# Kernel tuning notes

Hardware: AMD Instinct MI355X
Metric: run time of the kernel (lower is better)

## Reference

```python
import jax, jax.numpy as jnp
import numpy as np

NUM_CLS = 80
SR = 0.2
STRIDES = (8, 16, 32, 64, 128)
IMG = 1280
FMAPS = [(IMG // s, IMG // s) for s in STRIDES]
MAX_BOXES = 128
BIG_AREA = 1e7  # padding value for box-area argmin (matches tf.pad constant)


def _shrink_boxes(boxes, fw, fh, stride, sr):
    # shrink gt boxes by `sr` around their center and snap to feature-grid ints
    b = boxes / stride
    cx = (b[:, 0] + b[:, 2]) * 0.5
    cy = (b[:, 1] + b[:, 3]) * 0.5
    hw = (b[:, 2] - b[:, 0]) * sr * 0.5
    hh = (b[:, 3] - b[:, 1]) * sr * 0.5
    px1 = jnp.clip(jnp.floor(cx - hw), 0, fw - 1).astype(jnp.int32)
    py1 = jnp.clip(jnp.floor(cy - hh), 0, fh - 1).astype(jnp.int32)
    px2 = jnp.clip(jnp.ceil(cx + hw).astype(jnp.int32), px1 + 1, fw)
    py2 = jnp.clip(jnp.ceil(cy + hh).astype(jnp.int32), py1 + 1, fh)
    return px1, py1, px2, py2


def _level_targets(boxes, labels, valid, sel_w, fh, fw, stride):
    # Vectorized replacement of the per-box tf.map_fn + tf.pad + argmin + gather_nd.
    # The original builds a padded dense map per box; padding values are:
    #   cls one-hot -> 0, soft weight -> 1, regr mask -> 0, regr target -> 0, area -> 1e7.
    # We instead compute dense [K,fh,fw] maps and mask, which is the same math.
    px1, py1, px2, py2 = _shrink_boxes(boxes, fw, fh, stride, SR)  # [K]
    sx = (jnp.arange(fw, dtype=jnp.float32) + 0.5) * stride  # pixel-center x
    sy = (jnp.arange(fh, dtype=jnp.float32) + 0.5) * stride  # pixel-center y
    dl = jnp.maximum(sx[None, None, :] - boxes[:, 0, None, None], 0.0)  # [K,fh,fw]
    dt = jnp.maximum(sy[None, :, None] - boxes[:, 1, None, None], 0.0)
    dr = jnp.maximum(boxes[:, 2, None, None] - sx[None, None, :], 0.0)
    db = jnp.maximum(boxes[:, 3, None, None] - sy[None, :, None], 0.0)
    gx = jnp.arange(fw)[None, None, :]
    gy = jnp.arange(fh)[None, :, None]
    in_box = ((gx >= px1[:, None, None]) & (gx < px2[:, None, None])
              & (gy >= py1[:, None, None]) & (gy < py2[:, None, None])
              & valid[:, None, None])  # [K,fh,fw] positive region per box
    area = jnp.where(in_box, (dl + dr) * (dt + db), BIG_AREA)
    win = jnp.argmin(area, axis=0)  # [fh,fw] smallest-area box per pixel

    take = lambda a: jnp.take_along_axis(a, win[None], axis=0)[0]
    is_pos = take(in_box).astype(jnp.float32)
    dl_w, dt_w, dr_w, db_w = take(dl), take(dt), take(dr), take(db)

    # anchor-point weight min/max ratio (guard 0/0 which is only hit off-target)
    num = jnp.minimum(dl_w, dr_w) * jnp.minimum(dt_w, db_w)
    den = jnp.maximum(dl_w, dr_w) * jnp.maximum(dt_w, db_w)
    ap = jnp.where(den > 0, num / jnp.maximum(den, 1e-12), 0.0)
    soft = jnp.where(is_pos > 0, ap * sel_w[win], 1.0)

    onehot = jax.nn.one_hot(labels[win], NUM_CLS, dtype=jnp.float32) * is_pos[..., None]
    regr = (jnp.stack([dl_w, dt_w, dr_w, db_w], axis=-1) / (4.0 * stride)) * is_pos[..., None]
    extra = jnp.stack([soft, is_pos], axis=-1)  # [fh,fw,2] soft weight + pos mask
    cls_t = jnp.concatenate([onehot, extra], axis=-1).reshape(fh * fw, NUM_CLS + 2)
    regr_t = jnp.concatenate([regr, extra], axis=-1).reshape(fh * fw, 4 + 2)
    return cls_t, regr_t


def reference(gt_boxes, feature_select_weight, feature_maps_shape):
    # feature_maps_shape is accepted for signature fidelity; shapes must be
    # static under jit so we use the FMAPS constant (same values).
    labels = gt_boxes[:, 4].astype(jnp.int32)
    boxes = gt_boxes[:, :4]
    valid = jnp.any(jnp.abs(boxes) > 0, axis=1)  # trim_zero_padding_boxes as mask
    cls_list, regr_list = [], []
    for lvl, stride in enumerate(STRIDES):
        fh, fw = FMAPS[lvl]
        c, r = _level_targets(boxes, labels, valid,
                              feature_select_weight[:, lvl], fh, fw, stride)
        cls_list.append(c)
        regr_list.append(r)
    return jnp.concatenate(cls_list, axis=0), jnp.concatenate(regr_list, axis=0)


def setup_inputs():
    key = jax.random.key(0)
    k1, k2, k3, k4 = jax.random.split(key, 4)
    xy = jax.random.uniform(k1, (MAX_BOXES, 2), minval=0.0, maxval=IMG - 64.0)
    wh = jax.random.uniform(k2, (MAX_BOXES, 2), minval=32.0, maxval=420.0)
    x2y2 = jnp.minimum(xy + wh, IMG - 1.0)
    labels = jax.random.randint(k3, (MAX_BOXES, 1), 0, NUM_CLS).astype(jnp.float32)
    gt = jnp.concatenate([xy, x2y2, labels], axis=-1)
    # zero out last quarter to exercise the zero-padding trim path
    pad_mask = (jnp.arange(MAX_BOXES) < MAX_BOXES * 3 // 4).astype(jnp.float32)
    gt = gt * pad_mask[:, None]
    fsw = jax.random.uniform(k4, (MAX_BOXES, len(STRIDES)))
    fshape = jnp.array(FMAPS, dtype=jnp.int32)
    return {"gt_boxes": gt, "feature_select_weight": fsw,
            "feature_maps_shape": fshape}
```

## Files before the change

### kernel.cpp

```cpp
#include <hip/hip_runtime.h>
#include <math.h>

#define NUM_CLS   80
#define MAX_BOXES 128
#define NLVL      5
#define BIG_AREA  1.0e7f
#define TOTAL_PIX 34100

__global__ __launch_bounds__(256) void fcos_targets_kernel(
    const float* __restrict__ gt,
    const float* __restrict__ fsw,
    float* __restrict__ out_cls,
    float* __restrict__ out_reg)
{
    __shared__ float sbx[MAX_BOXES][4];
    __shared__ float ssw[MAX_BOXES][NLVL];
    __shared__ int   slab[MAX_BOXES];
    __shared__ unsigned char svalid[MAX_BOXES];

    const int t = threadIdx.x;
    if (t < MAX_BOXES) {
        float x1 = gt[t * 5 + 0];
        float y1 = gt[t * 5 + 1];
        float x2 = gt[t * 5 + 2];
        float y2 = gt[t * 5 + 3];
        sbx[t][0] = x1; sbx[t][1] = y1; sbx[t][2] = x2; sbx[t][3] = y2;
        slab[t]   = (int)gt[t * 5 + 4];
        svalid[t] = (fabsf(x1) > 0.f) || (fabsf(y1) > 0.f) ||
                    (fabsf(x2) > 0.f) || (fabsf(y2) > 0.f);
    } else {
        int b = t - MAX_BOXES;
        #pragma unroll
        for (int l = 0; l < NLVL; ++l) ssw[b][l] = fsw[b * NLVL + l];
    }
    __syncthreads();

    const int pid = blockIdx.x * 256 + t;
    if (pid >= TOTAL_PIX) return;

    int lvl, base, fw; float stride;
    if      (pid < 25600) { lvl = 0; base = 0;     fw = 160; stride = 8.f;   }
    else if (pid < 32000) { lvl = 1; base = 25600; fw = 80;  stride = 16.f;  }
    else if (pid < 33600) { lvl = 2; base = 32000; fw = 40;  stride = 32.f;  }
    else if (pid < 34000) { lvl = 3; base = 33600; fw = 20;  stride = 64.f;  }
    else                  { lvl = 4; base = 34000; fw = 10;  stride = 128.f; }

    const int lp = pid - base;
    const int gy = lp / fw;
    const int gx = lp - gy * fw;
    const float sx = ((float)gx + 0.5f) * stride;
    const float sy = ((float)gy + 0.5f) * stride;
    const float inv_s = 1.0f / stride;
    const float fwm1  = (float)(fw - 1);

    float best = BIG_AREA;
    int   win  = 0;
    for (int i = 0; i < MAX_BOXES; ++i) {
        const float x1 = sbx[i][0], y1 = sbx[i][1];
        const float x2 = sbx[i][2], y2 = sbx[i][3];

        const float bx1 = x1 * inv_s, by1 = y1 * inv_s;
        const float bx2 = x2 * inv_s, by2 = y2 * inv_s;
        const float cx = (bx1 + bx2) * 0.5f;
        const float cy = (by1 + by2) * 0.5f;
        const float hw = ((bx2 - bx1) * 0.2f) * 0.5f;
        const float hh = ((by2 - by1) * 0.2f) * 0.5f;
        const int px1 = (int)fminf(fmaxf(floorf(cx - hw), 0.f), fwm1);
        const int py1 = (int)fminf(fmaxf(floorf(cy - hh), 0.f), fwm1);
        const int px2 = min(max((int)ceilf(cx + hw), px1 + 1), fw);
        const int py2 = min(max((int)ceilf(cy + hh), py1 + 1), fw);

        const bool inb = (gx >= px1) & (gx < px2) &
                         (gy >= py1) & (gy < py2) & (svalid[i] != 0);

        const float dl = fmaxf(sx - x1, 0.f);
        const float dt = fmaxf(sy - y1, 0.f);
        const float dr = fmaxf(x2 - sx, 0.f);
        const float db = fmaxf(y2 - sy, 0.f);
        const float area = inb ? (dl + dr) * (dt + db) : BIG_AREA;
        if (area < best) { best = area; win = i; }
    }

    const float x1 = sbx[win][0], y1 = sbx[win][1];
    const float x2 = sbx[win][2], y2 = sbx[win][3];
    const float bx1 = x1 * inv_s, by1 = y1 * inv_s;
    const float bx2 = x2 * inv_s, by2 = y2 * inv_s;
    const float cx = (bx1 + bx2) * 0.5f;
    const float cy = (by1 + by2) * 0.5f;
    const float hw = ((bx2 - bx1) * 0.2f) * 0.5f;
    const float hh = ((by2 - by1) * 0.2f) * 0.5f;
    const int px1 = (int)fminf(fmaxf(floorf(cx - hw), 0.f), fwm1);
    const int py1 = (int)fminf(fmaxf(floorf(cy - hh), 0.f), fwm1);
    const int px2 = min(max((int)ceilf(cx + hw), px1 + 1), fw);
    const int py2 = min(max((int)ceilf(cy + hh), py1 + 1), fw);
    const bool inb = (gx >= px1) & (gx < px2) &
                     (gy >= py1) & (gy < py2) & (svalid[win] != 0);

    const float dl = fmaxf(sx - x1, 0.f);
    const float dt = fmaxf(sy - y1, 0.f);
    const float dr = fmaxf(x2 - sx, 0.f);
    const float db = fmaxf(y2 - sy, 0.f);

    const float is_pos = inb ? 1.0f : 0.0f;
    const float num = fminf(dl, dr) * fminf(dt, db);
    const float den = fmaxf(dl, dr) * fmaxf(dt, db);
    const float ap  = (den > 0.f) ? num / fmaxf(den, 1e-12f) : 0.0f;
    const float soft = inb ? ap * ssw[win][lvl] : 1.0f;
    const int   lab  = slab[win];

    float* crow = out_cls + (size_t)pid * (NUM_CLS + 2);
    #pragma unroll
    for (int c = 0; c < NUM_CLS; ++c) crow[c] = 0.0f;
    if (inb) crow[lab] = 1.0f;
    crow[NUM_CLS]     = soft;
    crow[NUM_CLS + 1] = is_pos;

    const float rs = (1.0f / 4.0f) * inv_s;
    float* rrow = out_reg + (size_t)pid * 6;
    rrow[0] = dl * rs * is_pos;
    rrow[1] = dt * rs * is_pos;
    rrow[2] = dr * rs * is_pos;
    rrow[3] = db * rs * is_pos;
    rrow[4] = soft;
    rrow[5] = is_pos;
}

extern "C" void kernel_launch(void* const* d_in, const int* in_sizes, int n_in,
                              void* d_out, int out_size, void* d_ws, size_t ws_size,
                              hipStream_t stream) {
    (void)in_sizes; (void)n_in; (void)out_size; (void)d_ws; (void)ws_size;
    const float* gt  = (const float*)d_in[0];
    const float* fsw = (const float*)d_in[1];
    float* out_cls = (float*)d_out;
    float* out_reg = out_cls + (size_t)TOTAL_PIX * (NUM_CLS + 2);

    const int threads = 256;
    const int blocks  = (TOTAL_PIX + threads - 1) / threads;
    fcos_targets_kernel<<<blocks, threads, 0, stream>>>(gt, fsw, out_cls, out_reg);
}
```

Before: 85.08 us.

## Precompute shrunk boxes per level, split box loop across threads, coalesce output stores

Each block now precomputes the shrunk integer box bounds for all five levels once into shared memory. The inner argmin loop no longer redoes the float divide, floor and ceil work per pixel. Two threads cooperate on each pixel, each scanning half the boxes, and the halves are merged through shared memory. Per-pixel results are staged in shared memory so the 82-wide class rows and 6-wide regression rows are written as coalesced float4 stores instead of strided scalar stores. In exchange the kernel adds extra barriers and twice as many blocks.

```diff
diff --git a/kernel.cpp b/kernel.cpp
--- a/kernel.cpp
+++ b/kernel.cpp
@@ -1,11 +1,13 @@
 #include <hip/hip_runtime.h>
 #include <math.h>
+#include <limits.h>
 
 #define NUM_CLS   80
 #define MAX_BOXES 128
 #define NLVL      5
 #define BIG_AREA  1.0e7f
 #define TOTAL_PIX 34100
+#define PPB       128
 
 __global__ __launch_bounds__(256) void fcos_targets_kernel(
     const float* __restrict__ gt,
@@ -13,116 +15,173 @@
     float* __restrict__ out_cls,
     float* __restrict__ out_reg)
 {
-    __shared__ float sbx[MAX_BOXES][4];
-    __shared__ float ssw[MAX_BOXES][NLVL];
-    __shared__ int   slab[MAX_BOXES];
-    __shared__ unsigned char svalid[MAX_BOXES];
+    __shared__ float4 sbx[MAX_BOXES];
+    __shared__ int4   sshr[MAX_BOXES][NLVL];
+    __shared__ float  ssw[MAX_BOXES][NLVL];
+    __shared__ int    slab[MAX_BOXES];
+    __shared__ float  pbest[PPB];
+    __shared__ int    pwin[PPB];
+    __shared__ float  st_soft[PPB];
+    __shared__ float  st_ispos[PPB];
+    __shared__ int    st_lab[PPB];
+    __shared__ float  st_reg[PPB][4];
 
     const int t = threadIdx.x;
+
     if (t < MAX_BOXES) {
-        float x1 = gt[t * 5 + 0];
-        float y1 = gt[t * 5 + 1];
-        float x2 = gt[t * 5 + 2];
-        float y2 = gt[t * 5 + 3];
-        sbx[t][0] = x1; sbx[t][1] = y1; sbx[t][2] = x2; sbx[t][3] = y2;
-        slab[t]   = (int)gt[t * 5 + 4];
-        svalid[t] = (fabsf(x1) > 0.f) || (fabsf(y1) > 0.f) ||
-                    (fabsf(x2) > 0.f) || (fabsf(y2) > 0.f);
+        const float x1 = gt[t * 5 + 0];
+        const float y1 = gt[t * 5 + 1];
+        const float x2 = gt[t * 5 + 2];
+        const float y2 = gt[t * 5 + 3];
+        sbx[t]  = make_float4(x1, y1, x2, y2);
+        slab[t] = (int)gt[t * 5 + 4];
+        const bool valid = (fabsf(x1) > 0.f) || (fabsf(y1) > 0.f) ||
+                           (fabsf(x2) > 0.f) || (fabsf(y2) > 0.f);
+        #pragma unroll
+        for (int l = 0; l < NLVL; ++l) {
+            const float inv_s = 1.0f / (float)(8 << l);
+            const int   fw    = 1280 >> (3 + l);
+            const float fwm1  = (float)(fw - 1);
+            const float bx1 = x1 * inv_s, by1 = y1 * inv_s;
+            const float bx2 = x2 * inv_s, by2 = y2 * inv_s;
+            const float cx = (bx1 + bx2) * 0.5f;
+            const float cy = (by1 + by2) * 0.5f;
+            const float hw = ((bx2 - bx1) * 0.2f) * 0.5f;
+            const float hh = ((by2 - by1) * 0.2f) * 0.5f;
+            int px1 = (int)fminf(fmaxf(floorf(cx - hw), 0.f), fwm1);
+            int py1 = (int)fminf(fmaxf(floorf(cy - hh), 0.f), fwm1);
+            int px2 = min(max((int)ceilf(cx + hw), px1 + 1), fw);
+            int py2 = min(max((int)ceilf(cy + hh), py1 + 1), fw);
+            if (!valid) { px1 = INT_MAX; py1 = INT_MAX; px2 = 0; py2 = 0; }
+            sshr[t][l] = make_int4(px1, py1, px2, py2);
+        }
     } else {
-        int b = t - MAX_BOXES;
+        const int b = t - MAX_BOXES;
         #pragma unroll
         for (int l = 0; l < NLVL; ++l) ssw[b][l] = fsw[b * NLVL + l];
     }
     __syncthreads();
 
-    const int pid = blockIdx.x * 256 + t;
-    if (pid >= TOTAL_PIX) return;
-
-    int lvl, base, fw; float stride;
-    if      (pid < 25600) { lvl = 0; base = 0;     fw = 160; stride = 8.f;   }
-    else if (pid < 32000) { lvl = 1; base = 25600; fw = 80;  stride = 16.f;  }
-    else if (pid < 33600) { lvl = 2; base = 32000; fw = 40;  stride = 32.f;  }
-    else if (pid < 34000) { lvl = 3; base = 33600; fw = 20;  stride = 64.f;  }
-    else                  { lvl = 4; base = 34000; fw = 10;  stride = 128.f; }
-
-    const int lp = pid - base;
-    const int gy = lp / fw;
-    const int gx = lp - gy * fw;
-    const float sx = ((float)gx + 0.5f) * stride;
-    const float sy = ((float)gy + 0.5f) * stride;
-    const float inv_s = 1.0f / stride;
-    const float fwm1  = (float)(fw - 1);
+    const int block_base = blockIdx.x * PPB;
+    const int count = min(PPB, TOTAL_PIX - block_base);
+    const int p   = t & (PPB - 1);
+    const int pid = block_base + p;
+    const bool active = (p < count);
 
     float best = BIG_AREA;
-    int   win  = 0;
-    for (int i = 0; i < MAX_BOXES; ++i) {
-        const float x1 = sbx[i][0], y1 = sbx[i][1];
-        const float x2 = sbx[i][2], y2 = sbx[i][3];
+    int   win  = (t < PPB) ? 0 : 64;
+    int   lvl = 0, fw = 160, gx = 0, gy = 0;
+    float sx = 0.f, sy = 0.f;
 
-        const float bx1 = x1 * inv_s, by1 = y1 * inv_s;
-        const float bx2 = x2 * inv_s, by2 = y2 * inv_s;
-        const float cx = (bx1 + bx2) * 0.5f;
-        const float cy = (by1 + by2) * 0.5f;
-        const float hw = ((bx2 - bx1) * 0.2f) * 0.5f;
-        const float hh = ((by2 - by1) * 0.2f) * 0.5f;
-        const int px1 = (int)fminf(fmaxf(floorf(cx - hw), 0.f), fwm1);
-        const int py1 = (int)fminf(fmaxf(floorf(cy - hh), 0.f), fwm1);
-        const int px2 = min(max((int)ceilf(cx + hw), px1 + 1), fw);
-        const int py2 = min(max((int)ceilf(cy + hh), py1 + 1), fw);
+    if (active) {
+        float stride;
+        if      (pid < 25600) { lvl = 0; fw = 160; const int lp = pid;         gy = lp / 160; gx = lp - gy * 160; stride = 8.f;   }
+        else if (pid < 32000) { lvl = 1; fw = 80;  const int lp = pid - 25600; gy = lp / 80;  gx = lp - gy * 80;  stride = 16.f;  }
+        else if (pid < 33600) { lvl = 2; fw = 40;  const int lp = pid - 32000; gy = lp / 40;  gx = lp - gy * 40;  stride = 32.f;  }
+        else if (pid < 34000) { lvl = 3; fw = 20;  const int lp = pid - 33600; gy = lp / 20;  gx = lp - gy * 20;  stride = 64.f;  }
+        else                  { lvl = 4; fw = 10;  const int lp = pid - 34000; gy = lp / 10;  gx = lp - gy * 10;  stride = 128.f; }
+        sx = ((float)gx + 0.5f) * stride;
+        sy = ((float)gy + 0.5f) * stride;
 
-        const bool inb = (gx >= px1) & (gx < px2) &
-                         (gy >= py1) & (gy < py2) & (svalid[i] != 0);
+        const int i0 = (t < PPB) ? 0 : 64;
+        for (int j = 0; j < 64; ++j) {
+            const int i = i0 + j;
+            const int4  s = sshr[i][lvl];
+            const float4 b = sbx[i];
+            const bool inb = (gx >= s.x) & (gx < s.z) & (gy >= s.y) & (gy < s.w);
+            const float dl = fmaxf(sx - b.x, 0.f);
+            const float dt = fmaxf(sy - b.y, 0.f);
+            const float dr = fmaxf(b.z - sx, 0.f);
+            const float db = fmaxf(b.w - sy, 0.f);
+            const float area = inb ? (dl + dr) * (dt + db) : BIG_AREA;
+            if (area < best) { best = area; win = i; }
+        }
+    }
+    if (t >= PPB) { pbest[p] = best; pwin[p] = win; }
+    __syncthreads();
 
-        const float dl = fmaxf(sx - x1, 0.f);
-        const float dt = fmaxf(sy - y1, 0.f);
-        const float dr = fmaxf(x2 - sx, 0.f);
-        const float db = fmaxf(y2 - sy, 0.f);
-        const float area = inb ? (dl + dr) * (dt + db) : BIG_AREA;
-        if (area < best) { best = area; win = i; }
+    if (t < PPB && active) {
+        const float b2 = pbest[p];
+        if (b2 < best) { best = b2; win = pwin[p]; }
+
+        const int4   s = sshr[win][lvl];
+        const float4 b = sbx[win];
+        const bool inb = (gx >= s.x) & (gx < s.z) & (gy >= s.y) & (gy < s.w);
+        const float dl = fmaxf(sx - b.x, 0.f);
+        const float dt = fmaxf(sy - b.y, 0.f);
+        const float dr = fmaxf(b.z - sx, 0.f);
+        const float db = fmaxf(b.w - sy, 0.f);
+
+        const float is_pos = inb ? 1.0f : 0.0f;
+        const float num = fminf(dl, dr) * fminf(dt, db);
+        const float den = fmaxf(dl, dr) * fmaxf(dt, db);
+        const float ap  = (den > 0.f) ? num / fmaxf(den, 1e-12f) : 0.0f;
+        const float soft = inb ? ap * ssw[win][lvl] : 1.0f;
+
+        const float rs = 0.25f / (float)(8 << lvl);
+        st_soft[p]  = soft;
+        st_ispos[p] = is_pos;
+        st_lab[p]   = slab[win];
+        st_reg[p][0] = dl * rs * is_pos;
+        st_reg[p][1] = dt * rs * is_pos;
+        st_reg[p][2] = dr * rs * is_pos;
+        st_reg[p][3] = db * rs * is_pos;
     }
+    __syncthreads();
 
-    const float x1 = sbx[win][0], y1 = sbx[win][1];
-    const float x2 = sbx[win][2], y2 = sbx[win][3];
-    const float bx1 = x1 * inv_s, by1 = y1 * inv_s;
-    const float bx2 = x2 * inv_s, by2 = y2 * inv_s;
-    const float cx = (bx1 + bx2) * 0.5f;
-    const float cy = (by1 + by2) * 0.5f;
-    const float hw = ((bx2 - bx1) * 0.2f) * 0.5f;
-    const float hh = ((by2 - by1) * 0.2f) * 0.5f;
-    const int px1 = (int)fminf(fmaxf(floorf(cx - hw), 0.f), fwm1);
-    const int py1 = (int)fminf(fmaxf(floorf(cy - hh), 0.f), fwm1);
-    const int px2 = min(max((int)ceilf(cx + hw), px1 + 1), fw);
-    const int py2 = min(max((int)ceilf(cy + hh), py1 + 1), fw);
-    const bool inb = (gx >= px1) & (gx < px2) &
-                     (gy >= py1) & (gy < py2) & (svalid[win] != 0);
-
-    const float dl = fmaxf(sx - x1, 0.f);
-    const float dt = fmaxf(sy - y1, 0.f);
-    const float dr = fmaxf(x2 - sx, 0.f);
-    const float db = fmaxf(y2 - sy, 0.f);
-
-    const float is_pos = inb ? 1.0f : 0.0f;
-    const float num = fminf(dl, dr) * fminf(dt, db);
-    const float den = fmaxf(dl, dr) * fmaxf(dt, db);
-    const float ap  = (den > 0.f) ? num / fmaxf(den, 1e-12f) : 0.0f;
-    const float soft = inb ? ap * ssw[win][lvl] : 1.0f;
-    const int   lab  = slab[win];
-
-    float* crow = out_cls + (size_t)pid * (NUM_CLS + 2);
-    #pragma unroll
-    for (int c = 0; c < NUM_CLS; ++c) crow[c] = 0.0f;
-    if (inb) crow[lab] = 1.0f;
-    crow[NUM_CLS]     = soft;
-    crow[NUM_CLS + 1] = is_pos;
-
-    const float rs = (1.0f / 4.0f) * inv_s;
-    float* rrow = out_reg + (size_t)pid * 6;
-    rrow[0] = dl * rs * is_pos;
-    rrow[1] = dt * rs * is_pos;
-    rrow[2] = dr * rs * is_pos;
-    rrow[3] = db * rs * is_pos;
-    rrow[4] = soft;
-    rrow[5] = is_pos;
+    if (count == PPB) {
+        float4* cp = (float4*)(out_cls + (size_t)block_base * (NUM_CLS + 2));
+        for (int q = t; q < PPB * (NUM_CLS + 2) / 4; q += 256) {
+            const int flat = q * 4;
+            const int row0 = (int)((unsigned)flat / 82u);
+            const int col0 = flat - row0 * 82;
+            float v[4];
+            #pragma unroll
+            for (int k = 0; k < 4; ++k) {
+                int r = row0, c = col0 + k;
+                if (c >= 82) { c -= 82; ++r; }
+                const float ip = st_ispos[r];
+                float val;
+                if (c < NUM_CLS)      val = (c == st_lab[r] && ip != 0.f) ? 1.0f : 0.0f;
+                else if (c == NUM_CLS) val = st_soft[r];
+                else                   val = ip;
+                v[k] = val;
+            }
+            cp[q] = make_float4(v[0], v[1], v[2], v[3]);
+        }
+        float4* rp = (float4*)(out_reg + (size_t)block_base * 6);
+        for (int q = t; q < PPB * 6 / 4; q += 256) {
+            const int flat = q * 4;
+            const int row0 = (int)((unsigned)flat / 6u);
+            const int col0 = flat - row0 * 6;
+            float v[4];
+            #pragma unroll
+            for (int k = 0; k < 4; ++k) {
+                int r = row0, c = col0 + k;
+                if (c >= 6) { c -= 6; ++r; }
+                v[k] = (c < 4) ? st_reg[r][c] : ((c == 4) ? st_soft[r] : st_ispos[r]);
+            }
+            rp[q] = make_float4(v[0], v[1], v[2], v[3]);
+        }
+    } else {
+        float* cbase = out_cls + (size_t)block_base * (NUM_CLS + 2);
+        for (int q = t; q < count * (NUM_CLS + 2); q += 256) {
+            const int r = (int)((unsigned)q / 82u);
+            const int c = q - r * 82;
+            const float ip = st_ispos[r];
+            float val;
+            if (c < NUM_CLS)       val = (c == st_lab[r] && ip != 0.f) ? 1.0f : 0.0f;
+            else if (c == NUM_CLS) val = st_soft[r];
+            else                   val = ip;
+            cbase[q] = val;
+        }
+        float* rbase = out_reg + (size_t)block_base * 6;
+        for (int q = t; q < count * 6; q += 256) {
+            const int r = (int)((unsigned)q / 6u);
+            const int c = q - r * 6;
+            rbase[q] = (c < 4) ? st_reg[r][c] : ((c == 4) ? st_soft[r] : st_ispos[r]);
+        }
+    }
 }
 
 extern "C" void kernel_launch(void* const* d_in, const int* in_sizes, int n_in,
@@ -134,7 +193,6 @@
     float* out_cls = (float*)d_out;
     float* out_reg = out_cls + (size_t)TOTAL_PIX * (NUM_CLS + 2);
 
-    const int threads = 256;
-    const int blocks  = (TOTAL_PIX + threads - 1) / threads;
-    fcos_targets_kernel<<<blocks, threads, 0, stream>>>(gt, fsw, out_cls, out_reg);
+    const int blocks = (TOTAL_PIX + PPB - 1) / PPB;
+    fcos_targets_kernel<<<blocks, 256, 0, stream>>>(gt, fsw, out_cls, out_reg);
 }
```

Result: faster. 71.46 us (-16.0%).

## Replace per-pixel box scan with box-driven atomicMin scatter over shrunk regions

Applied to the files above, without the earlier changes.

Instead of every pixel scanning all 128 boxes, each (box, level) thread walks only its shrunk positive region and does a 64-bit atomicMin on a packed (area bits, box index) key per pixel. A separate init kernel writes the default outputs with vectorized float4 stores and resets the keys, and a finalize kernel fills in only the pixels that have a winner. This removes the O(pixels×boxes) compute but adds three launches, a workspace buffer and atomics. Scatter parallelism is low (640 threads, serial loops over each region), and tie-breaking relies on the packed box index matching argmin's first-index rule.

```diff
diff --git a/kernel.cpp b/kernel.cpp
--- a/kernel.cpp
+++ b/kernel.cpp
@@ -1,88 +1,74 @@
 #include <hip/hip_runtime.h>
 #include <math.h>
+#include <limits.h>
 
 #define NUM_CLS   80
 #define MAX_BOXES 128
 #define NLVL      5
-#define BIG_AREA  1.0e7f
 #define TOTAL_PIX 34100
 
-__global__ __launch_bounds__(256) void fcos_targets_kernel(
+#define CLS_F4    699050
+#define REG_F4    51150
+#define KEY_U4    17050
+
+__global__ __launch_bounds__(256) void init_kernel(
+    float* __restrict__ out_cls, float* __restrict__ out_reg,
+    unsigned long long* __restrict__ keys)
+{
+    const int tid = blockIdx.x * 256 + threadIdx.x;
+    const int nth = gridDim.x * 256;
+
+    float4* cp = (float4*)out_cls;
+    for (int q = tid; q < CLS_F4; q += nth) {
+        const int flat = q * 4;
+        const int c0 = flat - ((int)((unsigned)flat / 82u)) * 82;
+        float4 v;
+        v.x = (c0     == 80) ? 1.f : 0.f;
+        v.y = (c0 + 1 == 80) ? 1.f : 0.f;
+        v.z = (c0 + 2 == 80) ? 1.f : 0.f;
+        v.w = (c0 + 3 == 80) ? 1.f : 0.f;
+        cp[q] = v;
+    }
+    float4* rp = (float4*)out_reg;
+    for (int q = tid; q < REG_F4; q += nth) {
+        const int flat = q * 4;
+        const int c0 = flat - ((int)((unsigned)flat / 6u)) * 6;
+        float4 v;
+        v.x = (c0     == 4) ? 1.f : 0.f;
+        v.y = (c0 + 1 == 4) ? 1.f : 0.f;
+        v.z = (c0 + 2 == 4) ? 1.f : 0.f;
+        v.w = (c0 + 3 == 4) ? 1.f : 0.f;
+        rp[q] = v;
+    }
+    uint4* kp = (uint4*)keys;
+    const uint4 ff = make_uint4(~0u, ~0u, ~0u, ~0u);
+    for (int q = tid; q < KEY_U4; q += nth) kp[q] = ff;
+}
+
+__global__ __launch_bounds__(256) void scatter_kernel(
     const float* __restrict__ gt,
-    const float* __restrict__ fsw,
-    float* __restrict__ out_cls,
-    float* __restrict__ out_reg)
+    unsigned long long* __restrict__ keys)
 {
-    __shared__ float sbx[MAX_BOXES][4];
-    __shared__ float ssw[MAX_BOXES][NLVL];
-    __shared__ int   slab[MAX_BOXES];
-    __shared__ unsigned char svalid[MAX_BOXES];
+    const int t = blockIdx.x * 256 + threadIdx.x;
+    if (t >= MAX_BOXES * NLVL) return;
+    const int box = t / NLVL;
+    const int lvl = t - box * NLVL;
 
-    const int t = threadIdx.x;
-    if (t < MAX_BOXES) {
-        float x1 = gt[t * 5 + 0];
-        float y1 = gt[t * 5 + 1];
-        float x2 = gt[t * 5 + 2];
-        float y2 = gt[t * 5 + 3];
-        sbx[t][0] = x1; sbx[t][1] = y1; sbx[t][2] = x2; sbx[t][3] = y2;
-        slab[t]   = (int)gt[t * 5 + 4];
-        svalid[t] = (fabsf(x1) > 0.f) || (fabsf(y1) > 0.f) ||
-                    (fabsf(x2) > 0.f) || (fabsf(y2) > 0.f);
-    } else {
-        int b = t - MAX_BOXES;
-        #pragma unroll
-        for (int l = 0; l < NLVL; ++l) ssw[b][l] = fsw[b * NLVL + l];
-    }
-    __syncthreads();
+    const float x1 = gt[box * 5 + 0];
+    const float y1 = gt[box * 5 + 1];
+    const float x2 = gt[box * 5 + 2];
+    const float y2 = gt[box * 5 + 3];
+    const bool valid = (fabsf(x1) > 0.f) || (fabsf(y1) > 0.f) ||
+                       (fabsf(x2) > 0.f) || (fabsf(y2) > 0.f);
+    if (!valid) return;
 
-    const int pid = blockIdx.x * 256 + t;
-    if (pid >= TOTAL_PIX) return;
+    const float stride = (float)(8 << lvl);
+    const float inv_s  = 1.0f / stride;
+    const int   fw     = 160 >> lvl;
+    const float fwm1   = (float)(fw - 1);
+    const int   base   = (lvl == 0) ? 0 : (lvl == 1) ? 25600 :
+                         (lvl == 2) ? 32000 : (lvl == 3) ? 33600 : 34000;
 
-    int lvl, base, fw; float stride;
-    if      (pid < 25600) { lvl = 0; base = 0;     fw = 160; stride = 8.f;   }
-    else if (pid < 32000) { lvl = 1; base = 25600; fw = 80;  stride = 16.f;  }
-    else if (pid < 33600) { lvl = 2; base = 32000; fw = 40;  stride = 32.f;  }
-    else if (pid < 34000) { lvl = 3; base = 33600; fw = 20;  stride = 64.f;  }
-    else                  { lvl = 4; base = 34000; fw = 10;  stride = 128.f; }
-
-    const int lp = pid - base;
-    const int gy = lp / fw;
-    const int gx = lp - gy * fw;
-    const float sx = ((float)gx + 0.5f) * stride;
-    const float sy = ((float)gy + 0.5f) * stride;
-    const float inv_s = 1.0f / stride;
-    const float fwm1  = (float)(fw - 1);
-
-    float best = BIG_AREA;
-    int   win  = 0;
-    for (int i = 0; i < MAX_BOXES; ++i) {
-        const float x1 = sbx[i][0], y1 = sbx[i][1];
-        const float x2 = sbx[i][2], y2 = sbx[i][3];
-
-        const float bx1 = x1 * inv_s, by1 = y1 * inv_s;
-        const float bx2 = x2 * inv_s, by2 = y2 * inv_s;
-        const float cx = (bx1 + bx2) * 0.5f;
-        const float cy = (by1 + by2) * 0.5f;
-        const float hw = ((bx2 - bx1) * 0.2f) * 0.5f;
-        const float hh = ((by2 - by1) * 0.2f) * 0.5f;
-        const int px1 = (int)fminf(fmaxf(floorf(cx - hw), 0.f), fwm1);
-        const int py1 = (int)fminf(fmaxf(floorf(cy - hh), 0.f), fwm1);
-        const int px2 = min(max((int)ceilf(cx + hw), px1 + 1), fw);
-        const int py2 = min(max((int)ceilf(cy + hh), py1 + 1), fw);
-
-        const bool inb = (gx >= px1) & (gx < px2) &
-                         (gy >= py1) & (gy < py2) & (svalid[i] != 0);
-
-        const float dl = fmaxf(sx - x1, 0.f);
-        const float dt = fmaxf(sy - y1, 0.f);
-        const float dr = fmaxf(x2 - sx, 0.f);
-        const float db = fmaxf(y2 - sy, 0.f);
-        const float area = inb ? (dl + dr) * (dt + db) : BIG_AREA;
-        if (area < best) { best = area; win = i; }
-    }
-
-    const float x1 = sbx[win][0], y1 = sbx[win][1];
-    const float x2 = sbx[win][2], y2 = sbx[win][3];
     const float bx1 = x1 * inv_s, by1 = y1 * inv_s;
     const float bx2 = x2 * inv_s, by2 = y2 * inv_s;
     const float cx = (bx1 + bx2) * 0.5f;
@@ -93,48 +79,92 @@
     const int py1 = (int)fminf(fmaxf(floorf(cy - hh), 0.f), fwm1);
     const int px2 = min(max((int)ceilf(cx + hw), px1 + 1), fw);
     const int py2 = min(max((int)ceilf(cy + hh), py1 + 1), fw);
-    const bool inb = (gx >= px1) & (gx < px2) &
-                     (gy >= py1) & (gy < py2) & (svalid[win] != 0);
+
+    for (int gy = py1; gy < py2; ++gy) {
+        const float sy = ((float)gy + 0.5f) * stride;
+        const float dt = fmaxf(sy - y1, 0.f);
+        const float db = fmaxf(y2 - sy, 0.f);
+        const float vsum = dt + db;
+        for (int gx = px1; gx < px2; ++gx) {
+            const float sx = ((float)gx + 0.5f) * stride;
+            const float dl = fmaxf(sx - x1, 0.f);
+            const float dr = fmaxf(x2 - sx, 0.f);
+            const float area = (dl + dr) * vsum;
+            const unsigned long long key =
+                ((unsigned long long)__float_as_uint(area) << 32) |
+                (unsigned long long)(unsigned)box;
+            atomicMin(&keys[base + gy * fw + gx], key);
+        }
+    }
+}
+
+__global__ __launch_bounds__(256) void finalize_kernel(
+    const float* __restrict__ gt, const float* __restrict__ fsw,
+    const unsigned long long* __restrict__ keys,
+    float* __restrict__ out_cls, float* __restrict__ out_reg)
+{
+    const int pid = blockIdx.x * 256 + threadIdx.x;
+    if (pid >= TOTAL_PIX) return;
+    const unsigned long long k = keys[pid];
+    if (k == ~0ull) return;
+
+    const int win = (int)(unsigned)(k & 0xffffffffu);
+
+    int lvl, fw, lp;
+    float stride;
+    if      (pid < 25600) { lvl = 0; fw = 160; lp = pid;         stride = 8.f;   }
+    else if (pid < 32000) { lvl = 1; fw = 80;  lp = pid - 25600; stride = 16.f;  }
+    else if (pid < 33600) { lvl = 2; fw = 40;  lp = pid - 32000; stride = 32.f;  }
+    else if (pid < 34000) { lvl = 3; fw = 20;  lp = pid - 33600; stride = 64.f;  }
+    else                  { lvl = 4; fw = 10;  lp = pid - 34000; stride = 128.f; }
+    const int gy = lp / fw;
+    const int gx = lp - gy * fw;
+    const float sx = ((float)gx + 0.5f) * stride;
+    const float sy = ((float)gy + 0.5f) * stride;
+
+    const float x1 = gt[win * 5 + 0];
+    const float y1 = gt[win * 5 + 1];
+    const float x2 = gt[win * 5 + 2];
+    const float y2 = gt[win * 5 + 3];
+    const int   lab = (int)gt[win * 5 + 4];
 
     const float dl = fmaxf(sx - x1, 0.f);
     const float dt = fmaxf(sy - y1, 0.f);
     const float dr = fmaxf(x2 - sx, 0.f);
     const float db = fmaxf(y2 - sy, 0.f);
 
-    const float is_pos = inb ? 1.0f : 0.0f;
     const float num = fminf(dl, dr) * fminf(dt, db);
     const float den = fmaxf(dl, dr) * fmaxf(dt, db);
     const float ap  = (den > 0.f) ? num / fmaxf(den, 1e-12f) : 0.0f;
-    const float soft = inb ? ap * ssw[win][lvl] : 1.0f;
-    const int   lab  = slab[win];
+    const float soft = ap * fsw[win * NLVL + lvl];
 
     float* crow = out_cls + (size_t)pid * (NUM_CLS + 2);
-    #pragma unroll
-    for (int c = 0; c < NUM_CLS; ++c) crow[c] = 0.0f;
-    if (inb) crow[lab] = 1.0f;
-    crow[NUM_CLS]     = soft;
-    crow[NUM_CLS + 1] = is_pos;
+    crow[lab]          = 1.0f;
+    crow[NUM_CLS]      = soft;
+    crow[NUM_CLS + 1]  = 1.0f;
 
-    const float rs = (1.0f / 4.0f) * inv_s;
+    const float rs = 0.25f / stride;
     float* rrow = out_reg + (size_t)pid * 6;
-    rrow[0] = dl * rs * is_pos;
-    rrow[1] = dt * rs * is_pos;
-    rrow[2] = dr * rs * is_pos;
-    rrow[3] = db * rs * is_pos;
+    rrow[0] = dl * rs;
+    rrow[1] = dt * rs;
+    rrow[2] = dr * rs;
+    rrow[3] = db * rs;
     rrow[4] = soft;
-    rrow[5] = is_pos;
+    rrow[5] = 1.0f;
 }
 
 extern "C" void kernel_launch(void* const* d_in, const int* in_sizes, int n_in,
                               void* d_out, int out_size, void* d_ws, size_t ws_size,
                               hipStream_t stream) {
-    (void)in_sizes; (void)n_in; (void)out_size; (void)d_ws; (void)ws_size;
+    (void)in_sizes; (void)n_in; (void)out_size; (void)ws_size;
     const float* gt  = (const float*)d_in[0];
     const float* fsw = (const float*)d_in[1];
     float* out_cls = (float*)d_out;
     float* out_reg = out_cls + (size_t)TOTAL_PIX * (NUM_CLS + 2);
+    unsigned long long* keys = (unsigned long long*)d_ws;
 
-    const int threads = 256;
-    const int blocks  = (TOTAL_PIX + threads - 1) / threads;
-    fcos_targets_kernel<<<blocks, threads, 0, stream>>>(gt, fsw, out_cls, out_reg);
+    init_kernel<<<1024, 256, 0, stream>>>(out_cls, out_reg, keys);
+    scatter_kernel<<<(MAX_BOXES * NLVL + 255) / 256, 256, 0, stream>>>(gt, keys);
+    finalize_kernel<<<(TOTAL_PIX + 255) / 256, 256, 0, stream>>>(gt, fsw, keys,
+                                                                 out_cls, out_reg);
 }
```

Measured after the change: 72.98 us. 1.17x faster.
